# Optimization experiments

Hardware: AMD Instinct MI355X
Metric: run time of the kernel (lower is better)

Reference implementation:

```python
import jax, jax.numpy as jnp
import numpy as np

T_STEPS = 64      # AR order p
MAX_T = 65536     # trajectory length
BATCH = 256       # number of sampled trajectories
STD = 0.3


def setup_inputs() -> dict:
    key = jax.random.key(0)
    k1, k2, k3 = jax.random.split(key, 3)
    raw = jax.random.normal(k1, (T_STEPS,), dtype=jnp.float32)
    # torch init: params / sum(|params|)
    params = raw / jnp.sum(jnp.abs(raw))
    bias = jax.random.uniform(k2, (1,), dtype=jnp.float32)
    noise = jax.random.normal(k3, (BATCH, MAX_T), dtype=jnp.float32)
    return {"params": params, "bias": bias, "noise": noise}


def _ar_means(params, bias, length):
    """AR(p) recurrence: mean_i = sum_k params[k] * x[i-1-k] + bias, x init = 0.
    State holds the last p values, most-recent-first (matches the reversed
    indexing inputs[i-1 : i-p-1 : -1] in the torch code)."""
    p = params.shape[0]

    def step(state, _):
        new = jnp.dot(state, params) + bias[0]
        state = jnp.concatenate([new[None], state[:-1]])
        return state, new

    init = jnp.zeros((p,), dtype=params.dtype)
    _, means = jax.lax.scan(step, init, None, length=length)
    return means  # [length]


def reference(params, bias, noise):
    # means of the Normal over the trajectory (deterministic, shared by batch)
    means = _ar_means(params, bias, noise.shape[1])  # [T]
    # reparameterized sample: actions = mean + std * eps, eps ~ N(0, 1)
    actions = means[None, :] + jnp.asarray(STD, noise.dtype) * noise  # [B, T]
    return actions
```

## Files before the change

kernel.cpp:

```cpp
#include <hip/hip_runtime.h>

#define T_LEN   65536
#define BATCH   256
#define P       64
#define BASE    4096
#define K1_THREADS 256
#define W_TILE  1024
#define BCHUNK  8
#define VOFF    65536

typedef float f4 __attribute__((ext_vector_type(4)));


__constant__ int SCH_DST[14] = { 2, 3, 4, 6, 5, 7, 8,10,12,14, 9,11,13,15};
__constant__ int SCH_SRC[14] = { 1, 2, 2, 3, 4, 6, 4, 5, 6, 7, 8,10,12,14};
__constant__ int SCH_DBL[14] = { 1, 0, 1, 1, 0, 0, 1, 1, 1, 1, 0, 0, 0, 0};
__constant__ int SCH_W[14]   = {192,256,128,192,256,256,64,192,128,192,256,256,256,256};

__global__ __launch_bounds__(K1_THREADS, 1) void ar_k1(const float* __restrict__ params,
                                                       float* __restrict__ R) {
    __shared__ __align__(16) float Rl[BASE];
    __shared__ float p[128];
    __shared__ float Wp[64][4];
    __shared__ __align__(16) float Vs[68];
    __shared__ __align__(16) float Vnode[16][68];
    __shared__ __align__(16) float Tn[8][256];
    __shared__ __align__(16) float Ts[256];
    const int tid = threadIdx.x;
    if (tid < 128) p[tid] = (tid < P) ? params[tid] : 0.f;
    __syncthreads();

    if (tid < 64) {
        float z = 0.f;
        const float pk = p[tid];
        #pragma unroll 1
        for (int t = 0; t < 64; ++t) {
            float y  = __shfl(z, 0) + 1.0f;
            float zn = __shfl_down(z, 1);
            if (tid == 63) zn = 0.f;
            z = fmaf(pk, y, zn);
            if (tid == 0) Rl[t] = y;
        }
    }
    __syncthreads();

    #pragma unroll 1
    for (int L = 64; L <= BASE / 2; L <<= 1) {
        {
            const int j = tid >> 2, c = tid & 3;
            const int mbase = c << 4;
            float w = 0.f;
            #pragma unroll
            for (int mm = 0; mm < 16; ++mm) {
                const int m = mbase + mm;
                w = fmaf(p[m + j], Rl[L - 1 - m], w);
            }
            Wp[j][c] = w;
        }
        __syncthreads();
        if (tid <= P) {
            const float wj  = (tid < P)
                ? (Wp[tid][0] + Wp[tid][1] + Wp[tid][2] + Wp[tid][3]) : 0.f;
            const float wm1 = (tid >= 1)
                ? (Wp[tid-1][0] + Wp[tid-1][1] + Wp[tid-1][2] + Wp[tid-1][3]) : 0.f;
            Vs[tid] = wj - wm1;
        }
        __syncthreads();
        if (tid < P) {
            const int tau = tid;
            float acc = Rl[tau];
            #pragma unroll
            for (int i = 0; i < P; ++i) {
                const int idx = (tau - i) > 0 ? (tau - i) : 0;
                const float v = (i <= tau) ? Vs[i] : 0.f;
                acc = fmaf(v, Rl[idx], acc);
            }
            Rl[L + tau] = acc;
        }
        {
            const f4* __restrict__ Rl4 = reinterpret_cast<const f4*>(Rl);
            f4* __restrict__ Rl4w = reinterpret_cast<f4*>(Rl);
            const f4* __restrict__ V4 = reinterpret_cast<const f4*>(Vs);
            const int nq = (L - 64) >> 2;
            #pragma unroll 1
            for (int q = tid; q < nq; q += K1_THREADS) {
                f4 w4[17];
                #pragma unroll
                for (int j = 0; j < 17; ++j) w4[j] = Rl4[q + j];
                float a0 = w4[16].x, a1 = w4[16].y, a2 = w4[16].z, a3 = w4[16].w;
                #pragma unroll
                for (int g = 0; g < 16; ++g) {
                    const f4 v  = V4[g];
                    const f4 hi = w4[16 - g];
                    const f4 lo = w4[15 - g];
                    a0 = fmaf(v.x, hi.x, a0); a1 = fmaf(v.x, hi.y, a1);
                    a2 = fmaf(v.x, hi.z, a2); a3 = fmaf(v.x, hi.w, a3);
                    a0 = fmaf(v.y, lo.w, a0); a1 = fmaf(v.y, hi.x, a1);
                    a2 = fmaf(v.y, hi.y, a2); a3 = fmaf(v.y, hi.z, a3);
                    a0 = fmaf(v.z, lo.z, a0); a1 = fmaf(v.z, lo.w, a1);
                    a2 = fmaf(v.z, hi.x, a2); a3 = fmaf(v.z, hi.y, a3);
                    a0 = fmaf(v.w, lo.y, a0); a1 = fmaf(v.w, lo.z, a1);
                    a2 = fmaf(v.w, lo.w, a2); a3 = fmaf(v.w, hi.x, a3);
                }
                const float v64 = Vs[64];
                a0 = fmaf(v64, w4[0].x, a0); a1 = fmaf(v64, w4[0].y, a1);
                a2 = fmaf(v64, w4[0].z, a2); a3 = fmaf(v64, w4[0].w, a3);
                f4 o; o.x = a0; o.y = a1; o.z = a2; o.w = a3;
                Rl4w[((L + 64) >> 2) + q] = o;
            }
        }
        __syncthreads();
    }

    #pragma unroll 1
    for (int j = tid; j < BASE / 4; j += K1_THREADS)
        reinterpret_cast<f4*>(R)[j] = reinterpret_cast<const f4*>(Rl)[j];

    Tn[1][tid] = Rl[3840 + tid];
    __syncthreads();
    {
        const int j = tid >> 2, c = tid & 3, mbase = c << 4;
        float w = 0.f;
        #pragma unroll
        for (int mm = 0; mm < 16; ++mm) {
            const int m = mbase + mm;
            w = fmaf(p[m + j], Tn[1][255 - m], w);
        }
        Wp[j][c] = w;
    }
    __syncthreads();
    if (tid <= P) {
        const float wj  = (tid < P)
            ? (Wp[tid][0] + Wp[tid][1] + Wp[tid][2] + Wp[tid][3]) : 0.f;
        const float wm1 = (tid >= 1)
            ? (Wp[tid-1][0] + Wp[tid-1][1] + Wp[tid-1][2] + Wp[tid-1][3]) : 0.f;
        Vnode[1][tid] = wj - wm1;
    }
    __syncthreads();

    #pragma unroll 1
    for (int s = 0; s < 14; ++s) {
        const int dst = SCH_DST[s], src = SCH_SRC[s], wd = SCH_W[s];
        const bool dbl = SCH_DBL[s] != 0;
        float* td = (dst <= 7) ? Tn[dst] : Ts;
        const float* tsrc = Tn[src];
        const float* Vsr  = Vnode[src];
        if (tid < wd) {
            const float* s0 = dbl ? (tsrc + 64) : (Rl + 3840);
            float acc = s0[tid];
            #pragma unroll
            for (int i = 0; i <= P; ++i)
                acc = fmaf(Vsr[i], s0[tid - i], acc);
            td[tid] = acc;
        }
        __syncthreads();
        {
            const int j = tid >> 2, c = tid & 3, mbase = c << 4;
            float w = 0.f;
            #pragma unroll
            for (int mm = 0; mm < 16; ++mm) {
                const int m = mbase + mm;
                w = fmaf(p[m + j], td[wd - 1 - m], w);
            }
            Wp[j][c] = w;
        }
        __syncthreads();
        if (tid <= P) {
            const float wj  = (tid < P)
                ? (Wp[tid][0] + Wp[tid][1] + Wp[tid][2] + Wp[tid][3]) : 0.f;
            const float wm1 = (tid >= 1)
                ? (Wp[tid-1][0] + Wp[tid-1][1] + Wp[tid-1][2] + Wp[tid-1][3]) : 0.f;
            Vnode[dst][tid] = wj - wm1;
        }
        __syncthreads();
    }

    #pragma unroll 1
    for (int j = tid; j < 15 * 80; j += K1_THREADS) {
        const int k = j / 80 + 1, i = j - (k - 1) * 80;
        if (i < 65) R[VOFF + k * 80 + i] = Vnode[k][i];
    }
}

__global__ __launch_bounds__(256) void ar_out_fused(const float* __restrict__ R,
                                                    const float* __restrict__ bias,
                                                    const float* __restrict__ noise,
                                                    float* __restrict__ out) {
    __shared__ __align__(16) float win[1088];
    __shared__ __align__(16) float Vl[68];
    const int tid  = threadIdx.x;
    const int tile = blockIdx.x & 63;
    const int bc   = blockIdx.x >> 6;
    const int t0   = tile * W_TILE;
    const float b  = bias[0];
    const int k    = t0 >> 12;
    const f4* __restrict__ Rg4 = reinterpret_cast<const f4*>(R);

    f4 rt;
    if (k == 0) {
        const f4 r = Rg4[(t0 >> 2) + tid];
        rt.x = b * r.x; rt.y = b * r.y; rt.z = b * r.z; rt.w = b * r.w;
    } else {
        const int tau0 = t0 & 4095;
        if (tid < 65) Vl[tid] = R[VOFF + k * 80 + tid];
        f4* __restrict__ win4 = reinterpret_cast<f4*>(win);
        for (int j4 = tid; j4 < 272; j4 += 256) {
            const int u = tau0 - 64 + 4 * j4;
            f4 v;
            if (u >= 0) v = Rg4[u >> 2];
            else { v.x = 0.f; v.y = 0.f; v.z = 0.f; v.w = 0.f; }
            win4[j4] = v;
        }
        __syncthreads();
        const f4* __restrict__ V4 = reinterpret_cast<const f4*>(Vl);
        f4 w4[17];
        #pragma unroll
        for (int j = 0; j < 17; ++j) w4[j] = win4[tid + j];
        float a0 = w4[16].x, a1 = w4[16].y, a2 = w4[16].z, a3 = w4[16].w;
        #pragma unroll
        for (int g = 0; g < 16; ++g) {
            const f4 v  = V4[g];
            const f4 hi = w4[16 - g];
            const f4 lo = w4[15 - g];
            a0 = fmaf(v.x, hi.x, a0); a1 = fmaf(v.x, hi.y, a1);
            a2 = fmaf(v.x, hi.z, a2); a3 = fmaf(v.x, hi.w, a3);
            a0 = fmaf(v.y, lo.w, a0); a1 = fmaf(v.y, hi.x, a1);
            a2 = fmaf(v.y, hi.y, a2); a3 = fmaf(v.y, hi.z, a3);
            a0 = fmaf(v.z, lo.z, a0); a1 = fmaf(v.z, lo.w, a1);
            a2 = fmaf(v.z, hi.x, a2); a3 = fmaf(v.z, hi.y, a3);
            a0 = fmaf(v.w, lo.y, a0); a1 = fmaf(v.w, lo.z, a1);
            a2 = fmaf(v.w, lo.w, a2); a3 = fmaf(v.w, hi.x, a3);
        }
        const float v64 = Vl[64];
        a0 = fmaf(v64, w4[0].x, a0); a1 = fmaf(v64, w4[0].y, a1);
        a2 = fmaf(v64, w4[0].z, a2); a3 = fmaf(v64, w4[0].w, a3);
        rt.x = b * a0; rt.y = b * a1; rt.z = b * a2; rt.w = b * a3;
    }

    const int nb4 = T_LEN >> 2;
    const int col = (t0 >> 2) + tid;
    const f4* __restrict__ n4 = reinterpret_cast<const f4*>(noise);
    f4* __restrict__ o4 = reinterpret_cast<f4*>(out);
    #pragma unroll
    for (int bi = 0; bi < BCHUNK; ++bi) {
        const int idx = (bc * BCHUNK + bi) * nb4 + col;
        const f4 n = __builtin_nontemporal_load(n4 + idx);
        f4 o;
        o.x = fmaf(0.3f, n.x, rt.x);
        o.y = fmaf(0.3f, n.y, rt.y);
        o.z = fmaf(0.3f, n.z, rt.z);
        o.w = fmaf(0.3f, n.w, rt.w);
        __builtin_nontemporal_store(o, o4 + idx);
    }
}

extern "C" void kernel_launch(void* const* d_in, const int* in_sizes, int n_in,
                              void* d_out, int out_size, void* d_ws, size_t ws_size,
                              hipStream_t stream) {
    const float* params = (const float*)d_in[0];
    const float* bias   = (const float*)d_in[1];
    const float* noise  = (const float*)d_in[2];
    float* out = (float*)d_out;
    float* R   = (float*)d_ws;

    hipLaunchKernelGGL(ar_k1, dim3(1), dim3(K1_THREADS), 0, stream, params, R);
    hipLaunchKernelGGL(ar_out_fused, dim3(64 * 32), dim3(256), 0, stream,
                       R, bias, noise, out);
}
```

Measured before the change: 167.5 us.

## Fuse AR prefix computation into output kernel, recomputing per block

Removes the single-block precompute kernel and workspace round-trip. Every output block now recomputes the 4096-step base response and only the jump-chain of V operators its tile needs, then combines with the noise. Noise loads are issued up front so they overlap with the redundant recurrence work, and the tap reduction is rewritten to use a warp shuffle instead of a shared scratch array. This trades one serial launch and a global sync for redundant compute in all 2048 blocks.

```diff
diff --git a/kernel.cpp b/kernel.cpp
--- a/kernel.cpp
+++ b/kernel.cpp
@@ -1,32 +1,87 @@
 #include <hip/hip_runtime.h>
 
 #define T_LEN   65536
-#define BATCH   256
 #define P       64
 #define BASE    4096
-#define K1_THREADS 256
 #define W_TILE  1024
 #define BCHUNK  8
-#define VOFF    65536
 
 typedef float f4 __attribute__((ext_vector_type(4)));
 
 
-__constant__ int SCH_DST[14] = { 2, 3, 4, 6, 5, 7, 8,10,12,14, 9,11,13,15};
-__constant__ int SCH_SRC[14] = { 1, 2, 2, 3, 4, 6, 4, 5, 6, 7, 8,10,12,14};
-__constant__ int SCH_DBL[14] = { 1, 0, 1, 1, 0, 0, 1, 1, 1, 1, 0, 0, 0, 0};
-__constant__ int SCH_W[14]   = {192,256,128,192,256,256,64,192,128,192,256,256,256,256};
-
-__global__ __launch_bounds__(K1_THREADS, 1) void ar_k1(const float* __restrict__ params,
-                                                       float* __restrict__ R) {
+__constant__ unsigned char CH_N[16] = {0,0,1,2,2,3,3,4,3,4,4,5,4,5,5,6};
+__constant__ unsigned char CH_DBL[16][6] = {
+  {0,0,0,0,0,0},{0,0,0,0,0,0},
+  {1,0,0,0,0,0},{1,0,0,0,0,0},
+  {1,1,0,0,0,0},{1,1,0,0,0,0},
+  {1,0,1,0,0,0},{1,0,1,0,0,0},
+  {1,1,1,0,0,0},{1,1,1,0,0,0},
+  {1,1,0,1,0,0},{1,1,0,1,0,0},
+  {1,0,1,1,0,0},{1,0,1,1,0,0},
+  {1,0,1,0,1,0},{1,0,1,0,1,0},
+};
+__constant__ unsigned short CH_W[16][6] = {
+  {0,0,0,0,0,0},{0,0,0,0,0,0},
+  {192,0,0,0,0,0},{192,256,0,0,0,0},
+  {192,128,0,0,0,0},{192,128,256,0,0,0},
+  {192,256,192,0,0,0},{192,256,192,256,0,0},
+  {192,128,64,0,0,0},{192,128,64,256,0,0},
+  {192,128,256,192,0,0},{192,128,256,192,256,0},
+  {192,256,192,128,0,0},{192,256,192,128,256,0},
+  {192,256,192,256,192,0},{192,256,192,256,192,256},
+};
+
+__device__ __forceinline__ void tapV(const float* __restrict__ td, int wd,
+                                     const float* __restrict__ p,
+                                     float* __restrict__ Vdst, int tid) {
+    if (tid < 64) {
+        const int j = tid;
+        float w0 = 0.f, w1 = 0.f, w2 = 0.f, w3 = 0.f;
+        #pragma unroll
+        for (int mm = 0; mm < 16; ++mm) w0 = fmaf(p[mm + j],      td[wd - 1  - mm], w0);
+        #pragma unroll
+        for (int mm = 0; mm < 16; ++mm) w1 = fmaf(p[16 + mm + j], td[wd - 17 - mm], w1);
+        #pragma unroll
+        for (int mm = 0; mm < 16; ++mm) w2 = fmaf(p[32 + mm + j], td[wd - 33 - mm], w2);
+        #pragma unroll
+        for (int mm = 0; mm < 16; ++mm) w3 = fmaf(p[48 + mm + j], td[wd - 49 - mm], w3);
+        const float wj  = ((w0 + w1) + w2) + w3;
+        const float wm1 = __shfl_up(wj, 1);
+        Vdst[j] = (j == 0) ? wj : (wj - wm1);
+        if (j == 63) Vdst[64] = 0.0f - wj;
+    }
+}
+
+__global__ __launch_bounds__(256) void ar_all(const float* __restrict__ params,
+                                              const float* __restrict__ bias,
+                                              const float* __restrict__ noise,
+                                              float* __restrict__ out) {
     __shared__ __align__(16) float Rl[BASE];
     __shared__ float p[128];
-    __shared__ float Wp[64][4];
-    __shared__ __align__(16) float Vs[68];
-    __shared__ __align__(16) float Vnode[16][68];
-    __shared__ __align__(16) float Tn[8][256];
-    __shared__ __align__(16) float Ts[256];
-    const int tid = threadIdx.x;
+    __shared__ __align__(16) float Va[68];
+    __shared__ __align__(16) float Vb[68];
+    __shared__ __align__(16) float Ta[256];
+    __shared__ __align__(16) float Tb[256];
+
+    const int tid  = threadIdx.x;
+    const int tile = blockIdx.x & 63;
+    const int bc   = blockIdx.x >> 6;
+    const int t0   = tile * W_TILE;
+    const int k    = t0 >> 12;
+    const int tau0 = t0 & 4095;
+    const int nb4  = T_LEN >> 2;
+    const int col  = (t0 >> 2) + tid;
+    const int row0 = bc * BCHUNK;
+    const f4* __restrict__ n4 = reinterpret_cast<const f4*>(noise);
+    f4* __restrict__ o4 = reinterpret_cast<f4*>(out);
+
+    f4 nf[BCHUNK];
+    #pragma unroll
+    for (int r = 0; r < BCHUNK; ++r)
+        nf[r] = __builtin_nontemporal_load(n4 + (row0 + r) * nb4 + col);
+
+    const float b = bias[0];
+
     if (tid < 128) p[tid] = (tid < P) ? params[tid] : 0.f;
     __syncthreads();
 
@@ -46,25 +101,7 @@
 
     #pragma unroll 1
     for (int L = 64; L <= BASE / 2; L <<= 1) {
-        {
-            const int j = tid >> 2, c = tid & 3;
-            const int mbase = c << 4;
-            float w = 0.f;
-            #pragma unroll
-            for (int mm = 0; mm < 16; ++mm) {
-                const int m = mbase + mm;
-                w = fmaf(p[m + j], Rl[L - 1 - m], w);
-            }
-            Wp[j][c] = w;
-        }
-        __syncthreads();
-        if (tid <= P) {
-            const float wj  = (tid < P)
-                ? (Wp[tid][0] + Wp[tid][1] + Wp[tid][2] + Wp[tid][3]) : 0.f;
-            const float wm1 = (tid >= 1)
-                ? (Wp[tid-1][0] + Wp[tid-1][1] + Wp[tid-1][2] + Wp[tid-1][3]) : 0.f;
-            Vs[tid] = wj - wm1;
-        }
+        tapV(Rl, L, p, Va, tid);
         __syncthreads();
         if (tid < P) {
             const int tau = tid;
@@ -72,7 +109,7 @@
             #pragma unroll
             for (int i = 0; i < P; ++i) {
                 const int idx = (tau - i) > 0 ? (tau - i) : 0;
-                const float v = (i <= tau) ? Vs[i] : 0.f;
+                const float v = (i <= tau) ? Va[i] : 0.f;
                 acc = fmaf(v, Rl[idx], acc);
             }
             Rl[L + tau] = acc;
@@ -80,10 +117,10 @@
         {
             const f4* __restrict__ Rl4 = reinterpret_cast<const f4*>(Rl);
             f4* __restrict__ Rl4w = reinterpret_cast<f4*>(Rl);
-            const f4* __restrict__ V4 = reinterpret_cast<const f4*>(Vs);
+            const f4* __restrict__ V4 = reinterpret_cast<const f4*>(Va);
             const int nq = (L - 64) >> 2;
             #pragma unroll 1
-            for (int q = tid; q < nq; q += K1_THREADS) {
+            for (int q = tid; q < nq; q += 256) {
                 f4 w4[17];
                 #pragma unroll
                 for (int j = 0; j < 17; ++j) w4[j] = Rl4[q + j];
@@ -102,7 +139,7 @@
                     a0 = fmaf(v.w, lo.y, a0); a1 = fmaf(v.w, lo.z, a1);
                     a2 = fmaf(v.w, lo.w, a2); a3 = fmaf(v.w, hi.x, a3);
                 }
-                const float v64 = Vs[64];
+                const float v64 = Va[64];
                 a0 = fmaf(v64, w4[0].x, a0); a1 = fmaf(v64, w4[0].y, a1);
                 a2 = fmaf(v64, w4[0].z, a2); a3 = fmaf(v64, w4[0].w, a3);
                 f4 o; o.x = a0; o.y = a1; o.z = a2; o.w = a3;
@@ -112,110 +149,49 @@
         __syncthreads();
     }
 
-    #pragma unroll 1
-    for (int j = tid; j < BASE / 4; j += K1_THREADS)
-        reinterpret_cast<f4*>(R)[j] = reinterpret_cast<const f4*>(Rl)[j];
-
-    Tn[1][tid] = Rl[3840 + tid];
-    __syncthreads();
-    {
-        const int j = tid >> 2, c = tid & 3, mbase = c << 4;
-        float w = 0.f;
-        #pragma unroll
-        for (int mm = 0; mm < 16; ++mm) {
-            const int m = mbase + mm;
-            w = fmaf(p[m + j], Tn[1][255 - m], w);
-        }
-        Wp[j][c] = w;
-    }
-    __syncthreads();
-    if (tid <= P) {
-        const float wj  = (tid < P)
-            ? (Wp[tid][0] + Wp[tid][1] + Wp[tid][2] + Wp[tid][3]) : 0.f;
-        const float wm1 = (tid >= 1)
-            ? (Wp[tid-1][0] + Wp[tid-1][1] + Wp[tid-1][2] + Wp[tid-1][3]) : 0.f;
-        Vnode[1][tid] = wj - wm1;
-    }
-    __syncthreads();
-
-    #pragma unroll 1
-    for (int s = 0; s < 14; ++s) {
-        const int dst = SCH_DST[s], src = SCH_SRC[s], wd = SCH_W[s];
-        const bool dbl = SCH_DBL[s] != 0;
-        float* td = (dst <= 7) ? Tn[dst] : Ts;
-        const float* tsrc = Tn[src];
-        const float* Vsr  = Vnode[src];
-        if (tid < wd) {
-            const float* s0 = dbl ? (tsrc + 64) : (Rl + 3840);
-            float acc = s0[tid];
-            #pragma unroll
-            for (int i = 0; i <= P; ++i)
-                acc = fmaf(Vsr[i], s0[tid - i], acc);
-            td[tid] = acc;
-        }
+    float* Vc = Va;
+    if (k >= 1) {
+        tapV(Rl + 3840, 256, p, Va, tid);
         __syncthreads();
-        {
-            const int j = tid >> 2, c = tid & 3, mbase = c << 4;
-            float w = 0.f;
-            #pragma unroll
-            for (int mm = 0; mm < 16; ++mm) {
-                const int m = mbase + mm;
-                w = fmaf(p[m + j], td[wd - 1 - m], w);
+        const float* Tp = Rl + 3840;
+        float* Tc = Ta;
+        const int ns = CH_N[k];
+        #pragma unroll 1
+        for (int s = 0; s < ns; ++s) {
+            const int wdn = (int)CH_W[k][s];
+            const float* s0 = CH_DBL[k][s] ? (Tp + 64) : (Rl + 3840);
+            if (tid < wdn) {
+                float acc = s0[tid];
+                #pragma unroll
+                for (int i = 0; i <= P; ++i)
+                    acc = fmaf(Vc[i], s0[tid - i], acc);
+                Tc[tid] = acc;
             }
-            Wp[j][c] = w;
-        }
-        __syncthreads();
-        if (tid <= P) {
-            const float wj  = (tid < P)
-                ? (Wp[tid][0] + Wp[tid][1] + Wp[tid][2] + Wp[tid][3]) : 0.f;
-            const float wm1 = (tid >= 1)
-                ? (Wp[tid-1][0] + Wp[tid-1][1] + Wp[tid-1][2] + Wp[tid-1][3]) : 0.f;
-            Vnode[dst][tid] = wj - wm1;
-        }
-        __syncthreads();
-    }
-
-    #pragma unroll 1
-    for (int j = tid; j < 15 * 80; j += K1_THREADS) {
-        const int k = j / 80 + 1, i = j - (k - 1) * 80;
-        if (i < 65) R[VOFF + k * 80 + i] = Vnode[k][i];
-    }
-}
-
-__global__ __launch_bounds__(256) void ar_out_fused(const float* __restrict__ R,
-                                                    const float* __restrict__ bias,
-                                                    const float* __restrict__ noise,
-                                                    float* __restrict__ out) {
-    __shared__ __align__(16) float win[1088];
-    __shared__ __align__(16) float Vl[68];
-    const int tid  = threadIdx.x;
-    const int tile = blockIdx.x & 63;
-    const int bc   = blockIdx.x >> 6;
-    const int t0   = tile * W_TILE;
-    const float b  = bias[0];
-    const int k    = t0 >> 12;
-    const f4* __restrict__ Rg4 = reinterpret_cast<const f4*>(R);
-
+            __syncthreads();
+            float* Vn = (Vc == Va) ? Vb : Va;
+            tapV(Tc, wdn, p, Vn, tid);
+            __syncthreads();
+            Vc = Vn; Tp = Tc; Tc = (Tc == Ta) ? Tb : Ta;
+        }
+    }
+
+    const f4* __restrict__ Rl4 = reinterpret_cast<const f4*>(Rl);
     f4 rt;
     if (k == 0) {
-        const f4 r = Rg4[(t0 >> 2) + tid];
+        const f4 r = Rl4[(t0 >> 2) + tid];
         rt.x = b * r.x; rt.y = b * r.y; rt.z = b * r.z; rt.w = b * r.w;
     } else {
-        const int tau0 = t0 & 4095;
-        if (tid < 65) Vl[tid] = R[VOFF + k * 80 + tid];
-        f4* __restrict__ win4 = reinterpret_cast<f4*>(win);
-        for (int j4 = tid; j4 < 272; j4 += 256) {
-            const int u = tau0 - 64 + 4 * j4;
+        const int wb = ((tau0 - 64) >> 2) + tid;
+        f4 w4[17];
+        #pragma unroll
+        for (int j = 0; j < 17; ++j) {
+            const int ix = wb + j;
             f4 v;
-            if (u >= 0) v = Rg4[u >> 2];
+            if (ix >= 0) v = Rl4[ix];
             else { v.x = 0.f; v.y = 0.f; v.z = 0.f; v.w = 0.f; }
-            win4[j4] = v;
-        }
-        __syncthreads();
-        const f4* __restrict__ V4 = reinterpret_cast<const f4*>(Vl);
-        f4 w4[17];
-        #pragma unroll
-        for (int j = 0; j < 17; ++j) w4[j] = win4[tid + j];
+            w4[j] = v;
+        }
+        const f4* __restrict__ V4 = reinterpret_cast<const f4*>(Vc);
         float a0 = w4[16].x, a1 = w4[16].y, a2 = w4[16].z, a3 = w4[16].w;
         #pragma unroll
         for (int g = 0; g < 16; ++g) {
@@ -231,26 +207,21 @@
             a0 = fmaf(v.w, lo.y, a0); a1 = fmaf(v.w, lo.z, a1);
             a2 = fmaf(v.w, lo.w, a2); a3 = fmaf(v.w, hi.x, a3);
         }
-        const float v64 = Vl[64];
+        const float v64 = Vc[64];
         a0 = fmaf(v64, w4[0].x, a0); a1 = fmaf(v64, w4[0].y, a1);
         a2 = fmaf(v64, w4[0].z, a2); a3 = fmaf(v64, w4[0].w, a3);
         rt.x = b * a0; rt.y = b * a1; rt.z = b * a2; rt.w = b * a3;
     }
 
-    const int nb4 = T_LEN >> 2;
-    const int col = (t0 >> 2) + tid;
-    const f4* __restrict__ n4 = reinterpret_cast<const f4*>(noise);
-    f4* __restrict__ o4 = reinterpret_cast<f4*>(out);
     #pragma unroll
-    for (int bi = 0; bi < BCHUNK; ++bi) {
-        const int idx = (bc * BCHUNK + bi) * nb4 + col;
-        const f4 n = __builtin_nontemporal_load(n4 + idx);
+    for (int r = 0; r < BCHUNK; ++r) {
+        const f4 n = nf[r];
         f4 o;
         o.x = fmaf(0.3f, n.x, rt.x);
         o.y = fmaf(0.3f, n.y, rt.y);
         o.z = fmaf(0.3f, n.z, rt.z);
         o.w = fmaf(0.3f, n.w, rt.w);
-        __builtin_nontemporal_store(o, o4 + idx);
+        __builtin_nontemporal_store(o, o4 + (row0 + r) * nb4 + col);
     }
 }
 
@@ -261,9 +232,8 @@
     const float* bias   = (const float*)d_in[1];
     const float* noise  = (const float*)d_in[2];
     float* out = (float*)d_out;
-    float* R   = (float*)d_ws;
-
-    hipLaunchKernelGGL(ar_k1, dim3(1), dim3(K1_THREADS), 0, stream, params, R);
-    hipLaunchKernelGGL(ar_out_fused, dim3(64 * 32), dim3(256), 0, stream,
-                       R, bias, noise, out);
+    (void)d_ws; (void)ws_size;
+
+    hipLaunchKernelGGL(ar_all, dim3(64 * 32), dim3(256), 0, stream,
+                       params, bias, noise, out);
 }
```

Result: slower. 369.6 us (+120.6%).

## Replace doubling recurrence with polynomial-power tree using companion reduction matrix

Applied to the files above, without the earlier changes.

Rewrites the single-block setup kernel. It now builds powers of the AR companion polynomial as a product tree of 65-coefficient polynomials, reduced modulo the characteristic polynomial through a precomputed 64x64 reduction table. This yields per-segment correction vectors directly, replacing the serial doubling-plus-schedule chain. The base impulse response shrinks to 2048 entries and the output kernel indexes segments at 2048 granularity. The intent is to shorten the serial latency of the one-block setup kernel, at the cost of more polynomial multiplications and new numerical error from the reduction.

```diff
diff --git a/kernel.cpp b/kernel.cpp
--- a/kernel.cpp
+++ b/kernel.cpp
@@ -1,33 +1,66 @@
 #include <hip/hip_runtime.h>
 
 #define T_LEN   65536
-#define BATCH   256
 #define P       64
-#define BASE    4096
+#define BASE    2048
 #define K1_THREADS 256
 #define W_TILE  1024
 #define BCHUNK  8
-#define VOFF    65536
+#define VOFF    4096
 
 typedef float f4 __attribute__((ext_vector_type(4)));
 
 
-__constant__ int SCH_DST[14] = { 2, 3, 4, 6, 5, 7, 8,10,12,14, 9,11,13,15};
-__constant__ int SCH_SRC[14] = { 1, 2, 2, 3, 4, 6, 4, 5, 6, 7, 8,10,12,14};
-__constant__ int SCH_DBL[14] = { 1, 0, 1, 1, 0, 0, 1, 1, 1, 1, 0, 0, 0, 0};
-__constant__ int SCH_W[14]   = {192,256,128,192,256,256,64,192,128,192,256,256,256,256};
+__constant__ unsigned char PRD_D[61] = {
+   2,
+   3, 4,
+   5, 6, 7, 8,
+   9,10,11,12,13,14,15,16,
+  17,18,19,20,21,22,23,24,25,26,27,28,29,30,31,32,
+  34,
+  35,36,
+  37,38,39,40,
+  41,42,43,44,45,46,47,48,
+  49,50,51,52,53,54,55,56,57,58,59,60,61,62,63
+};
+__constant__ unsigned char PRD_A[61] = {
+   1,
+   2, 2,
+   3, 3, 4, 4,
+   5, 5, 6, 6, 7, 7, 8, 8,
+   9, 9,10,10,11,11,12,12,13,13,14,14,15,15,16,16,
+  32,
+  34,34,
+  35,35,36,36,
+  37,37,38,38,39,39,40,40,
+  41,41,42,42,43,43,44,44,45,45,46,46,47,47,48
+};
+__constant__ unsigned char PRD_B[61] = {
+   1,
+   1, 2,
+   2, 3, 3, 4,
+   4, 5, 5, 6, 6, 7, 7, 8,
+   8, 9, 9,10,10,11,11,12,12,13,13,14,14,15,15,16,
+  32,
+  32,34,
+  34,35,35,36,
+  36,37,37,38,38,39,39,40,
+  40,41,41,42,42,43,43,44,44,45,45,46,46,47,47
+};
+__constant__ int STG[11] = {0,1,3,7,15,31,32,34,38,46,61};
 
 __global__ __launch_bounds__(K1_THREADS, 1) void ar_k1(const float* __restrict__ params,
                                                        float* __restrict__ R) {
+    __shared__ float p[128];
     __shared__ __align__(16) float Rl[BASE];
-    __shared__ float p[128];
-    __shared__ float Wp[64][4];
-    __shared__ __align__(16) float Vs[68];
-    __shared__ __align__(16) float Vnode[16][68];
-    __shared__ __align__(16) float Tn[8][256];
-    __shared__ __align__(16) float Ts[256];
+    __shared__ float T[64][68];
+    __shared__ float PL[64][68];
+    __shared__ float rawb[16][132];
+    __shared__ float Cs[32][68];
     const int tid = threadIdx.x;
+
     if (tid < 128) p[tid] = (tid < P) ? params[tid] : 0.f;
+    if (tid < 68)  PL[1][tid] = (tid == 64) ? 1.f : 0.f;
     __syncthreads();
 
     if (tid < 64) {
@@ -41,145 +74,91 @@
             z = fmaf(pk, y, zn);
             if (tid == 0) Rl[t] = y;
         }
-    }
-    __syncthreads();
-
-    #pragma unroll 1
-    for (int L = 64; L <= BASE / 2; L <<= 1) {
-        {
-            const int j = tid >> 2, c = tid & 3;
-            const int mbase = c << 4;
-            float w = 0.f;
+    } else if (tid < 128) {
+        const int l = tid - 64;
+        const float mc   = (l == 0) ? -p[63] : (p[64 - l] - p[63 - l]);
+        const float mc64 = 1.f + p[0];
+        float cur = mc, hi = mc64;
+        T[0][l] = cur; if (l == 0) T[0][64] = hi;
+        #pragma unroll 1
+        for (int j = 1; j < 64; ++j) {
+            const float up  = __shfl_up(cur, 1);
+            const float c63 = __shfl(cur, 63);
+            const float ncur = fmaf(hi, mc, (l == 0) ? 0.f : up);
+            hi  = fmaf(hi, mc64, c63);
+            cur = ncur;
+            T[j][l] = cur; if (l == 0) T[j][64] = hi;
+        }
+    }
+    __syncthreads();
+
+    #pragma unroll 1
+    for (int s = 0; s < 10; ++s) {
+        const int off = STG[s];
+        const int w   = STG[s + 1] - off;
+        #pragma unroll 1
+        for (int idx = tid; idx < w * 129; idx += K1_THREADS) {
+            const int pr = idx / 129, d = idx - pr * 129;
+            const float* __restrict__ A = PL[PRD_A[off + pr]];
+            const float* __restrict__ B = PL[PRD_B[off + pr]];
+            float acc = 0.f;
             #pragma unroll
-            for (int mm = 0; mm < 16; ++mm) {
-                const int m = mbase + mm;
-                w = fmaf(p[m + j], Rl[L - 1 - m], w);
+            for (int i = 0; i < 65; ++i) {
+                const int j  = d - i;
+                const int jc = j < 0 ? 0 : (j > 64 ? 64 : j);
+                const float bv = (j == jc) ? B[jc] : 0.f;
+                acc = fmaf(A[i], bv, acc);
             }
-            Wp[j][c] = w;
+            rawb[pr][d] = acc;
         }
         __syncthreads();
-        if (tid <= P) {
-            const float wj  = (tid < P)
-                ? (Wp[tid][0] + Wp[tid][1] + Wp[tid][2] + Wp[tid][3]) : 0.f;
-            const float wm1 = (tid >= 1)
-                ? (Wp[tid-1][0] + Wp[tid-1][1] + Wp[tid-1][2] + Wp[tid-1][3]) : 0.f;
-            Vs[tid] = wj - wm1;
+        #pragma unroll 1
+        for (int idx = tid; idx < w * 65; idx += K1_THREADS) {
+            const int pr = idx / 65, th = idx - pr * 65;
+            float r = rawb[pr][th];
+            #pragma unroll
+            for (int j = 0; j < 64; ++j)
+                r = fmaf(rawb[pr][65 + j], T[j][th], r);
+            PL[PRD_D[off + pr]][th] = r;
         }
         __syncthreads();
-        if (tid < P) {
-            const int tau = tid;
-            float acc = Rl[tau];
-            #pragma unroll
-            for (int i = 0; i < P; ++i) {
-                const int idx = (tau - i) > 0 ? (tau - i) : 0;
-                const float v = (i <= tau) ? Vs[i] : 0.f;
-                acc = fmaf(v, Rl[idx], acc);
-            }
-            Rl[L + tau] = acc;
-        }
-        {
-            const f4* __restrict__ Rl4 = reinterpret_cast<const f4*>(Rl);
-            f4* __restrict__ Rl4w = reinterpret_cast<f4*>(Rl);
-            const f4* __restrict__ V4 = reinterpret_cast<const f4*>(Vs);
-            const int nq = (L - 64) >> 2;
-            #pragma unroll 1
-            for (int q = tid; q < nq; q += K1_THREADS) {
-                f4 w4[17];
-                #pragma unroll
-                for (int j = 0; j < 17; ++j) w4[j] = Rl4[q + j];
-                float a0 = w4[16].x, a1 = w4[16].y, a2 = w4[16].z, a3 = w4[16].w;
-                #pragma unroll
-                for (int g = 0; g < 16; ++g) {
-                    const f4 v  = V4[g];
-                    const f4 hi = w4[16 - g];
-                    const f4 lo = w4[15 - g];
-                    a0 = fmaf(v.x, hi.x, a0); a1 = fmaf(v.x, hi.y, a1);
-                    a2 = fmaf(v.x, hi.z, a2); a3 = fmaf(v.x, hi.w, a3);
-                    a0 = fmaf(v.y, lo.w, a0); a1 = fmaf(v.y, hi.x, a1);
-                    a2 = fmaf(v.y, hi.y, a2); a3 = fmaf(v.y, hi.z, a3);
-                    a0 = fmaf(v.z, lo.z, a0); a1 = fmaf(v.z, lo.w, a1);
-                    a2 = fmaf(v.z, hi.x, a2); a3 = fmaf(v.z, hi.y, a3);
-                    a0 = fmaf(v.w, lo.y, a0); a1 = fmaf(v.w, lo.z, a1);
-                    a2 = fmaf(v.w, lo.w, a2); a3 = fmaf(v.w, hi.x, a3);
-                }
-                const float v64 = Vs[64];
-                a0 = fmaf(v64, w4[0].x, a0); a1 = fmaf(v64, w4[0].y, a1);
-                a2 = fmaf(v64, w4[0].z, a2); a3 = fmaf(v64, w4[0].w, a3);
-                f4 o; o.x = a0; o.y = a1; o.z = a2; o.w = a3;
-                Rl4w[((L + 64) >> 2) + q] = o;
-            }
-        }
-        __syncthreads();
-    }
-
-    #pragma unroll 1
-    for (int j = tid; j < BASE / 4; j += K1_THREADS)
-        reinterpret_cast<f4*>(R)[j] = reinterpret_cast<const f4*>(Rl)[j];
-
-    Tn[1][tid] = Rl[3840 + tid];
-    __syncthreads();
-    {
-        const int j = tid >> 2, c = tid & 3, mbase = c << 4;
-        float w = 0.f;
-        #pragma unroll
-        for (int mm = 0; mm < 16; ++mm) {
-            const int m = mbase + mm;
-            w = fmaf(p[m + j], Tn[1][255 - m], w);
-        }
-        Wp[j][c] = w;
-    }
-    __syncthreads();
-    if (tid <= P) {
-        const float wj  = (tid < P)
-            ? (Wp[tid][0] + Wp[tid][1] + Wp[tid][2] + Wp[tid][3]) : 0.f;
-        const float wm1 = (tid >= 1)
-            ? (Wp[tid-1][0] + Wp[tid-1][1] + Wp[tid-1][2] + Wp[tid-1][3]) : 0.f;
-        Vnode[1][tid] = wj - wm1;
-    }
-    __syncthreads();
-
-    #pragma unroll 1
-    for (int s = 0; s < 14; ++s) {
-        const int dst = SCH_DST[s], src = SCH_SRC[s], wd = SCH_W[s];
-        const bool dbl = SCH_DBL[s] != 0;
-        float* td = (dst <= 7) ? Tn[dst] : Ts;
-        const float* tsrc = Tn[src];
-        const float* Vsr  = Vnode[src];
-        if (tid < wd) {
-            const float* s0 = dbl ? (tsrc + 64) : (Rl + 3840);
-            float acc = s0[tid];
-            #pragma unroll
-            for (int i = 0; i <= P; ++i)
-                acc = fmaf(Vsr[i], s0[tid - i], acc);
-            td[tid] = acc;
-        }
-        __syncthreads();
-        {
-            const int j = tid >> 2, c = tid & 3, mbase = c << 4;
-            float w = 0.f;
-            #pragma unroll
-            for (int mm = 0; mm < 16; ++mm) {
-                const int m = mbase + mm;
-                w = fmaf(p[m + j], td[wd - 1 - m], w);
-            }
-            Wp[j][c] = w;
-        }
-        __syncthreads();
-        if (tid <= P) {
-            const float wj  = (tid < P)
-                ? (Wp[tid][0] + Wp[tid][1] + Wp[tid][2] + Wp[tid][3]) : 0.f;
-            const float wm1 = (tid >= 1)
-                ? (Wp[tid-1][0] + Wp[tid-1][1] + Wp[tid-1][2] + Wp[tid-1][3]) : 0.f;
-            Vnode[dst][tid] = wj - wm1;
-        }
-        __syncthreads();
-    }
-
-    #pragma unroll 1
-    for (int j = tid; j < 15 * 80; j += K1_THREADS) {
-        const int k = j / 80 + 1, i = j - (k - 1) * 80;
-        if (i < 65) R[VOFF + k * 80 + i] = Vnode[k][i];
-    }
+    }
+
+    #pragma unroll 1
+    for (int idx = tid; idx < 62 * 65; idx += K1_THREADS) {
+        const int row = idx / 65, th = idx - row * 65;
+        const int isV = row >= 31;
+        const int k   = isV ? (row - 30) : (row + 1);
+        const float* __restrict__ X = PL[isV ? ((k == 1) ? 32 : 32 + k) : k];
+        float cpo = (th == 64) ? X[0] : 0.f;
+        #pragma unroll
+        for (int j = 0; j < 64; ++j)
+            cpo = fmaf(X[j + 1], T[j][th], cpo);
+        const int i = 64 - th;
+        if (isV) R[VOFF + 80 * k + i] = cpo - ((i == 0) ? 1.f : 0.f);
+        else     Cs[k][i] = cpo;
+    }
+    __syncthreads();
+
+    #pragma unroll 1
+    for (int idx = tid; idx < 31 * 64; idx += K1_THREADS) {
+        const int kp = 1 + (idx >> 6), x = idx & 63;
+        const float* __restrict__ C = Cs[kp];
+        float acc = 0.f;
+        #pragma unroll
+        for (int i = 0; i <= P; ++i) {
+            const int u  = x - i;
+            const int uc = u < 0 ? 0 : u;
+            const float rv = (u >= 0) ? Rl[uc] : 0.f;
+            acc = fmaf(C[i], rv, acc);
+        }
+        Rl[64 * kp + x] = acc;
+    }
+    __syncthreads();
+
+    #pragma unroll 1
+    for (int j4 = tid; j4 < BASE / 4; j4 += K1_THREADS)
+        reinterpret_cast<f4*>(R)[j4] = reinterpret_cast<const f4*>(Rl)[j4];
 }
 
 __global__ __launch_bounds__(256) void ar_out_fused(const float* __restrict__ R,
@@ -193,7 +172,7 @@
     const int bc   = blockIdx.x >> 6;
     const int t0   = tile * W_TILE;
     const float b  = bias[0];
-    const int k    = t0 >> 12;
+    const int k    = t0 >> 11;
     const f4* __restrict__ Rg4 = reinterpret_cast<const f4*>(R);
 
     f4 rt;
@@ -201,7 +180,7 @@
         const f4 r = Rg4[(t0 >> 2) + tid];
         rt.x = b * r.x; rt.y = b * r.y; rt.z = b * r.z; rt.w = b * r.w;
     } else {
-        const int tau0 = t0 & 4095;
+        const int tau0 = t0 & 2047;
         if (tid < 65) Vl[tid] = R[VOFF + k * 80 + tid];
         f4* __restrict__ win4 = reinterpret_cast<f4*>(win);
         for (int j4 = tid; j4 < 272; j4 += 256) {
```

Result: slower. 246.4 us (+47.1%).

## Compute tap vectors per wavefront and process tree levels in parallel across waves

Applied to the files above, without the earlier changes.

The tap-vector computation moves into a single-wavefront helper that reduces with shuffles instead of a shared partial-sum array plus an extra barrier. The 14-step serial node schedule is regrouped into 6 dependency levels, with each wavefront handling one independent node per level. This cuts the number of block-wide barriers in the serial setup kernel and runs independent nodes concurrently. In exchange, each wave serially loops over up to 256 outputs, and the reordered schedule must still respect node dependencies.

```diff
diff --git a/kernel.cpp b/kernel.cpp
--- a/kernel.cpp
+++ b/kernel.cpp
@@ -1,7 +1,6 @@
 #include <hip/hip_runtime.h>
 
 #define T_LEN   65536
-#define BATCH   256
 #define P       64
 #define BASE    4096
 #define K1_THREADS 256
@@ -12,20 +11,39 @@
 typedef float f4 __attribute__((ext_vector_type(4)));
 
 
-__constant__ int SCH_DST[14] = { 2, 3, 4, 6, 5, 7, 8,10,12,14, 9,11,13,15};
-__constant__ int SCH_SRC[14] = { 1, 2, 2, 3, 4, 6, 4, 5, 6, 7, 8,10,12,14};
-__constant__ int SCH_DBL[14] = { 1, 0, 1, 1, 0, 0, 1, 1, 1, 1, 0, 0, 0, 0};
-__constant__ int SCH_W[14]   = {192,256,128,192,256,256,64,192,128,192,256,256,256,256};
+__constant__ unsigned char  TL_DST[14] = {2, 3,4, 6,5,8, 7,10,12,9, 14,11,13, 15};
+__constant__ unsigned char  TL_SRC[14] = {1, 2,2, 3,4,4, 6,5,6,8, 7,10,12, 14};
+__constant__ unsigned char  TL_DBL[14] = {1, 0,1, 1,0,1, 0,1,1,0, 1,0,0, 0};
+__constant__ unsigned short TL_W[14]   = {192, 256,128, 192,256,64, 256,192,128,256, 192,256,256, 256};
+__constant__ unsigned char  TL_OFF[7]  = {0,1,3,6,10,13,14};
+
+__device__ __forceinline__ void tapV_wave(const float* __restrict__ td, int wd,
+                                          const float* __restrict__ p,
+                                          float* __restrict__ Vdst, int lane) {
+    const int j = lane;
+    float w0 = 0.f, w1 = 0.f, w2 = 0.f, w3 = 0.f;
+    #pragma unroll
+    for (int mm = 0; mm < 16; ++mm) w0 = fmaf(p[mm + j],      td[wd - 1  - mm], w0);
+    #pragma unroll
+    for (int mm = 0; mm < 16; ++mm) w1 = fmaf(p[16 + mm + j], td[wd - 17 - mm], w1);
+    #pragma unroll
+    for (int mm = 0; mm < 16; ++mm) w2 = fmaf(p[32 + mm + j], td[wd - 33 - mm], w2);
+    #pragma unroll
+    for (int mm = 0; mm < 16; ++mm) w3 = fmaf(p[48 + mm + j], td[wd - 49 - mm], w3);
+    const float wj  = ((w0 + w1) + w2) + w3;
+    const float wm1 = __shfl_up(wj, 1);
+    Vdst[j] = (j == 0) ? wj : (wj - wm1);
+    if (j == 63) Vdst[64] = 0.0f - wj;
+}
 
 __global__ __launch_bounds__(K1_THREADS, 1) void ar_k1(const float* __restrict__ params,
                                                        float* __restrict__ R) {
     __shared__ __align__(16) float Rl[BASE];
     __shared__ float p[128];
-    __shared__ float Wp[64][4];
     __shared__ __align__(16) float Vs[68];
     __shared__ __align__(16) float Vnode[16][68];
     __shared__ __align__(16) float Tn[8][256];
-    __shared__ __align__(16) float Ts[256];
+    __shared__ __align__(16) float Tw[4][256];
     const int tid = threadIdx.x;
     if (tid < 128) p[tid] = (tid < P) ? params[tid] : 0.f;
     __syncthreads();
@@ -46,25 +64,7 @@
 
     #pragma unroll 1
     for (int L = 64; L <= BASE / 2; L <<= 1) {
-        {
-            const int j = tid >> 2, c = tid & 3;
-            const int mbase = c << 4;
-            float w = 0.f;
-            #pragma unroll
-            for (int mm = 0; mm < 16; ++mm) {
-                const int m = mbase + mm;
-                w = fmaf(p[m + j], Rl[L - 1 - m], w);
-            }
-            Wp[j][c] = w;
-        }
-        __syncthreads();
-        if (tid <= P) {
-            const float wj  = (tid < P)
-                ? (Wp[tid][0] + Wp[tid][1] + Wp[tid][2] + Wp[tid][3]) : 0.f;
-            const float wm1 = (tid >= 1)
-                ? (Wp[tid-1][0] + Wp[tid-1][1] + Wp[tid-1][2] + Wp[tid-1][3]) : 0.f;
-            Vs[tid] = wj - wm1;
-        }
+        if (tid < 64) tapV_wave(Rl, L, p, Vs, tid);
         __syncthreads();
         if (tid < P) {
             const int tau = tid;
@@ -113,65 +113,37 @@
     }
 
     #pragma unroll 1
-    for (int j = tid; j < BASE / 4; j += K1_THREADS)
-        reinterpret_cast<f4*>(R)[j] = reinterpret_cast<const f4*>(Rl)[j];
-
-    Tn[1][tid] = Rl[3840 + tid];
+    for (int j4 = tid; j4 < BASE / 4; j4 += K1_THREADS)
+        reinterpret_cast<f4*>(R)[j4] = reinterpret_cast<const f4*>(Rl)[j4];
+
+    if (tid < 64) tapV_wave(Rl + 3840, 256, p, Vnode[1], tid);
     __syncthreads();
-    {
-        const int j = tid >> 2, c = tid & 3, mbase = c << 4;
-        float w = 0.f;
-        #pragma unroll
-        for (int mm = 0; mm < 16; ++mm) {
-            const int m = mbase + mm;
-            w = fmaf(p[m + j], Tn[1][255 - m], w);
-        }
-        Wp[j][c] = w;
-    }
-    __syncthreads();
-    if (tid <= P) {
-        const float wj  = (tid < P)
-            ? (Wp[tid][0] + Wp[tid][1] + Wp[tid][2] + Wp[tid][3]) : 0.f;
-        const float wm1 = (tid >= 1)
-            ? (Wp[tid-1][0] + Wp[tid-1][1] + Wp[tid-1][2] + Wp[tid-1][3]) : 0.f;
-        Vnode[1][tid] = wj - wm1;
-    }
-    __syncthreads();
-
-    #pragma unroll 1
-    for (int s = 0; s < 14; ++s) {
-        const int dst = SCH_DST[s], src = SCH_SRC[s], wd = SCH_W[s];
-        const bool dbl = SCH_DBL[s] != 0;
-        float* td = (dst <= 7) ? Tn[dst] : Ts;
-        const float* tsrc = Tn[src];
-        const float* Vsr  = Vnode[src];
-        if (tid < wd) {
-            const float* s0 = dbl ? (tsrc + 64) : (Rl + 3840);
-            float acc = s0[tid];
-            #pragma unroll
-            for (int i = 0; i <= P; ++i)
-                acc = fmaf(Vsr[i], s0[tid - i], acc);
-            td[tid] = acc;
-        }
-        __syncthreads();
-        {
-            const int j = tid >> 2, c = tid & 3, mbase = c << 4;
-            float w = 0.f;
-            #pragma unroll
-            for (int mm = 0; mm < 16; ++mm) {
-                const int m = mbase + mm;
-                w = fmaf(p[m + j], td[wd - 1 - m], w);
+
+    #pragma unroll 1
+    for (int lvl = 0; lvl < 6; ++lvl) {
+        const int w = tid >> 6, lane = tid & 63;
+        const int n0 = TL_OFF[lvl], n1 = TL_OFF[lvl + 1];
+        const int e = n0 + w;
+        float* td = nullptr;
+        int wd = 0;
+        if (e < n1) {
+            const int dst = TL_DST[e], src = TL_SRC[e];
+            wd = TL_W[e];
+            const float* __restrict__ Vsr = Vnode[src];
+            const float* tail = (src == 1) ? (Rl + 3840) : Tn[src];
+            const float* s0 = TL_DBL[e] ? (tail + 64) : (Rl + 3840);
+            td = (dst <= 7) ? Tn[dst] : Tw[w];
+            #pragma unroll 1
+            for (int x = lane; x < wd; x += 64) {
+                float acc = s0[x];
+                #pragma unroll
+                for (int i = 0; i <= P; ++i)
+                    acc = fmaf(Vsr[i], s0[x - i], acc);
+                td[x] = acc;
             }
-            Wp[j][c] = w;
-        }
-        __syncthreads();
-        if (tid <= P) {
-            const float wj  = (tid < P)
-                ? (Wp[tid][0] + Wp[tid][1] + Wp[tid][2] + Wp[tid][3]) : 0.f;
-            const float wm1 = (tid >= 1)
-                ? (Wp[tid-1][0] + Wp[tid-1][1] + Wp[tid-1][2] + Wp[tid-1][3]) : 0.f;
-            Vnode[dst][tid] = wj - wm1;
-        }
+        }
+        __syncthreads();
+        if (e < n1) tapV_wave(td, wd, p, Vnode[TL_DST[e]], lane);
         __syncthreads();
     }
 
```

New measurement: 162.3 us. 3.1% less time.
